# Kernel optimization log

Measured on AMD Instinct MI355X. Metric: run time of the kernel, lower is better.

## Reference

```python
import jax, jax.numpy as jnp
import numpy as np


def setup_inputs() -> dict:
    key = jax.random.key(0)
    x = jax.random.normal(key, (4, 512, 64, 64), dtype=jnp.float32)
    return {"x": x}


def reference(x) -> jnp.ndarray:
    B, C, H, W = x.shape
    N = H * W
    v = x.reshape(B, C, N)                      # proj_query/key/value all = x flattened
    # energy[b, i, j] = sum_c x[b,c,i] * x[b,c,j]
    energy = jnp.einsum('bci,bcj->bij', v, v)
    attention = jax.nn.softmax(energy, axis=-1)  # softmax over last dim (keys j)
    # out[b,c,i] = sum_j v[b,c,j] * attention[b,i,j]  (== V @ attention^T)
    out = jnp.einsum('bcj,bij->bci', v, attention)
    return out.reshape(B, C, H, W)
```

## Files before the change

### kernel.cpp

```cpp
#include <hip/hip_runtime.h>
#include <hip/hip_bf16.h>

typedef unsigned short u16;
typedef unsigned int   u32;
typedef unsigned long long u64;
typedef __attribute__((ext_vector_type(8))) short bf16x8;
typedef __attribute__((ext_vector_type(4))) float f32x4;

#define BB 4
#define CC 512
#define NN 4096
#define LOG2E 1.44269504f

static __device__ __forceinline__ u16 f2b(float f) {
    __hip_bfloat16 h = __float2bfloat16(f);
    return *(u16*)&h;
}
static __device__ __forceinline__ u16 f2b_fast(float f) {
    u32 u = __builtin_bit_cast(u32, f);
    return (u16)((u + 0x8000u) >> 16);
}
static __device__ __forceinline__ float b2f(u16 b) {
    u32 u = (u32)b << 16;
    return __builtin_bit_cast(float, u);
}

typedef __attribute__((address_space(1))) const u32 GU32;
typedef __attribute__((address_space(3))) u32 LU32;
__device__ __forceinline__ void async16(const void* g, void* l) {
    __builtin_amdgcn_global_load_lds((GU32*)g, (LU32*)l, 16, 0, 0);
}

__global__ __launch_bounds__(256) void prep_kernel(const float* __restrict__ x,
                                                   u16* __restrict__ XT,
                                                   u16* __restrict__ XN,
                                                   float* __restrict__ norms,
                                                   int* __restrict__ maxn) {
    __shared__ __align__(8) u16 tile[64][68];
    __shared__ float nsum[64];
    int blk = blockIdx.x;
    int b  = blk >> 6;
    int n0 = (blk & 63) << 6;
    int t  = threadIdx.x;
    if (t < 64) nsum[t] = 0.f;

    int nq    = t & 15;
    int rbase = t >> 4;
    float psum[4] = {0.f, 0.f, 0.f, 0.f};

    for (int c0 = 0; c0 < CC; c0 += 64) {
        #pragma unroll
        for (int p = 0; p < 4; ++p) {
            int cl = p * 16 + rbase;
            const float* src = x + ((size_t)(b * CC + c0 + cl) * NN) + n0 + nq * 4;
            float4 v = *(const float4*)src;
            psum[0] += v.x * v.x; psum[1] += v.y * v.y;
            psum[2] += v.z * v.z; psum[3] += v.w * v.w;
            u64 pk = (u64)f2b(v.x) | ((u64)f2b(v.y) << 16) |
                     ((u64)f2b(v.z) << 32) | ((u64)f2b(v.w) << 48);
            *(u64*)&XN[((size_t)(b * CC + c0 + cl) * NN) + n0 + nq * 4] = pk;
            *(u64*)&tile[cl][nq * 4] = pk;
        }
        __syncthreads();
        int c2 = (t & 31) * 2;
        int nb = t >> 5;
        #pragma unroll
        for (int rr = 0; rr < 8; ++rr) {
            int nl = rr * 8 + nb;
            u32 val = (u32)tile[c2][nl] | ((u32)tile[c2 + 1][nl] << 16);
            *(u32*)&XT[((size_t)(b * NN + n0 + nl) * CC) + c0 + c2] = val;
        }
        __syncthreads();
    }
    #pragma unroll
    for (int k = 0; k < 4; ++k) atomicAdd(&nsum[nq * 4 + k], psum[k]);
    __syncthreads();
    if (t < 64) {
        float v = nsum[t];
        norms[(size_t)b * NN + n0 + t] = v;
        float m = v;
        #pragma unroll
        for (int d = 1; d < 64; d <<= 1) m = fmaxf(m, __shfl_xor(m, d));
        if (t == 0) atomicMax(&maxn[b], __float_as_int(m));
    }
}

__global__ __launch_bounds__(256, 2) void flash_kernel(const u16* __restrict__ XT,
                                                       const u16* __restrict__ XN,
                                                       const float* __restrict__ norms,
                                                       const int* __restrict__ maxn,
                                                       float* __restrict__ outF,
                                                       u16* __restrict__ outH,
                                                       float* __restrict__ l0g,
                                                       float* __restrict__ l1g,
                                                       int split) {
    __shared__ __align__(16) u16 KtT[2][32 * 520];
    __shared__ __align__(16) u16 Plds[2][64 * 40];
    __shared__ float lLds[64];

    int blk   = blockIdx.x;
    int inner = blk & 255;
    int hf    = split ? (blk >> 8) : 0;
    int xcd = inner & 7;
    int b   = xcd >> 1;
    int ib  = (inner >> 3) + ((xcd & 1) << 5);
    int i_base = ib * 64;
    int jlo = hf * (NN / 2) * split;
    int njt = split ? 64 : 128;

    int t    = threadIdx.x;
    int w    = t >> 6;
    int lane = t & 63;
    int l15  = lane & 15;
    int q    = lane >> 4;

    const u16* xtb = XT + (size_t)b * NN * CC;
    const u16* xnb = XN + (size_t)b * CC * NN;

    float mxn = __int_as_float(maxn[b]);
    float M2[4];
    #pragma unroll
    for (int r = 0; r < 4; ++r) {
        float nr = norms[(size_t)b * NN + i_base + w * 16 + q * 4 + r];
        M2[r] = (sqrtf(nr * mxn) - 40.f) * LOG2E;
    }

    bf16x8 qf[16];
    {
        const u16* qrow = xtb + (size_t)(i_base + w * 16 + l15) * CC;
        #pragma unroll
        for (int kk = 0; kk < 16; ++kk)
            qf[kk] = *(const bf16x8*)(qrow + kk * 32 + q * 8);
    }

    f32x4 o[8][4];
    #pragma unroll
    for (int ct = 0; ct < 8; ++ct)
        #pragma unroll
        for (int it = 0; it < 4; ++it)
            o[ct][it] = (f32x4){0.f, 0.f, 0.f, 0.f};
    float lpart[4] = {0.f, 0.f, 0.f, 0.f};

    {
        const u16* src = xtb + (size_t)(jlo + w * 8) * CC + lane * 8;
        #pragma unroll
        for (int rr = 0; rr < 8; ++rr)
            async16(src + rr * CC, &KtT[0][(w * 8 + rr) * 520]);
    }
    __syncthreads();

    for (int jt = 0; jt < njt; ++jt) {
        int buf = jt & 1;
        int j0  = jlo + jt * 32;

        bf16x8 vf[8];
        #pragma unroll
        for (int ct = 0; ct < 8; ++ct)
            vf[ct] = *(const bf16x8*)(xnb + (size_t)(w * 128 + ct * 16 + l15) * NN + j0 + q * 8);

        if (jt + 1 < njt) {
            const u16* src = xtb + (size_t)(j0 + 32 + w * 8) * CC + lane * 8;
            #pragma unroll
            for (int rr = 0; rr < 8; ++rr)
                async16(src + rr * CC, &KtT[buf ^ 1][(w * 8 + rr) * 520]);
        }

        f32x4 s0 = {0.f,0.f,0.f,0.f}, s1 = {0.f,0.f,0.f,0.f};
        #pragma unroll
        for (int kk = 0; kk < 16; ++kk) {
            bf16x8 b0 = *(const bf16x8*)&KtT[buf][(l15)      * 520 + kk * 32 + q * 8];
            bf16x8 b1 = *(const bf16x8*)&KtT[buf][(16 + l15) * 520 + kk * 32 + q * 8];
            s0 = __builtin_amdgcn_mfma_f32_16x16x32_bf16(qf[kk], b0, s0, 0, 0, 0);
            s1 = __builtin_amdgcn_mfma_f32_16x16x32_bf16(qf[kk], b1, s1, 0, 0, 0);
        }

        #pragma unroll
        for (int r = 0; r < 4; ++r) {
            float p0 = __builtin_amdgcn_exp2f(fmaf(s0[r], LOG2E, -M2[r]));
            float p1 = __builtin_amdgcn_exp2f(fmaf(s1[r], LOG2E, -M2[r]));
            u16 h0 = f2b_fast(p0), h1 = f2b_fast(p1);
            lpart[r] += b2f(h0) + b2f(h1);
            int row = w * 16 + q * 4 + r;
            Plds[buf][row * 40 +      l15] = h0;
            Plds[buf][row * 40 + 16 + l15] = h1;
        }
        __syncthreads();

        bf16x8 pb[4];
        #pragma unroll
        for (int it = 0; it < 4; ++it)
            pb[it] = *(const bf16x8*)&Plds[buf][(it * 16 + l15) * 40 + q * 8];
        #pragma unroll
        for (int ct = 0; ct < 8; ++ct)
            #pragma unroll
            for (int it = 0; it < 4; ++it)
                o[ct][it] = __builtin_amdgcn_mfma_f32_16x16x32_bf16(vf[ct], pb[it], o[ct][it], 0, 0, 0);
    }

    #pragma unroll
    for (int r = 0; r < 4; ++r) {
        float s = lpart[r];
        s += __shfl_xor(s, 1);
        s += __shfl_xor(s, 2);
        s += __shfl_xor(s, 4);
        s += __shfl_xor(s, 8);
        lpart[r] = s;
    }

    if (!split) {
        if (l15 == 0) {
            #pragma unroll
            for (int r = 0; r < 4; ++r) lLds[w * 16 + q * 4 + r] = lpart[r];
        }
        __syncthreads();
        float linv[4];
        #pragma unroll
        for (int it = 0; it < 4; ++it) linv[it] = 1.f / lLds[it * 16 + l15];
        float* ob = outF + (size_t)b * CC * NN;
        #pragma unroll
        for (int ct = 0; ct < 8; ++ct)
            #pragma unroll
            for (int r = 0; r < 4; ++r) {
                int c = w * 128 + ct * 16 + q * 4 + r;
                float* orow = ob + (size_t)c * NN + i_base;
                #pragma unroll
                for (int it = 0; it < 4; ++it)
                    orow[it * 16 + l15] = o[ct][it][r] * linv[it];
            }
    } else {
        if (l15 == 0) {
            float* lg = (hf == 0) ? l0g : l1g;
            #pragma unroll
            for (int r = 0; r < 4; ++r)
                lg[(size_t)b * NN + i_base + w * 16 + q * 4 + r] = lpart[r];
        }
        if (hf == 0) {
            float* ob = outF + (size_t)b * CC * NN;
            #pragma unroll
            for (int ct = 0; ct < 8; ++ct)
                #pragma unroll
                for (int r = 0; r < 4; ++r) {
                    int c = w * 128 + ct * 16 + q * 4 + r;
                    float* orow = ob + (size_t)c * NN + i_base;
                    #pragma unroll
                    for (int it = 0; it < 4; ++it)
                        orow[it * 16 + l15] = o[ct][it][r];
                }
        } else {
            u16* ob = outH + (size_t)b * CC * NN;
            #pragma unroll
            for (int ct = 0; ct < 8; ++ct)
                #pragma unroll
                for (int r = 0; r < 4; ++r) {
                    int c = w * 128 + ct * 16 + q * 4 + r;
                    u16* orow = ob + (size_t)c * NN + i_base;
                    #pragma unroll
                    for (int it = 0; it < 4; ++it)
                        orow[it * 16 + l15] = f2b(o[ct][it][r]);
                }
        }
    }
}

__global__ __launch_bounds__(256) void combine_kernel(float* __restrict__ out,
                                                      const u16* __restrict__ P1,
                                                      const float* __restrict__ l0,
                                                      const float* __restrict__ l1) {
    size_t g = (size_t)blockIdx.x * 256 + threadIdx.x;
    size_t f = g * 4;
    int i = (int)(f & (NN - 1));
    int b = (int)(f >> 21);
    float4 p0 = *(float4*)&out[f];
    u64 pk = *(const u64*)&P1[f];
    float p0a[4] = {p0.x, p0.y, p0.z, p0.w};
    float r[4];
    #pragma unroll
    for (int k = 0; k < 4; ++k) {
        float l = l0[(size_t)b * NN + i + k] + l1[(size_t)b * NN + i + k];
        float p1f = b2f((u16)((pk >> (16 * k)) & 0xFFFFu));
        r[k] = (p0a[k] + p1f) / l;
    }
    *(float4*)&out[f] = (float4){r[0], r[1], r[2], r[3]};
}

extern "C" void kernel_launch(void* const* d_in, const int* in_sizes, int n_in,
                              void* d_out, int out_size, void* d_ws, size_t ws_size,
                              hipStream_t stream) {
    const float* x = (const float*)d_in[0];
    size_t SZ = (size_t)BB * NN * CC;
    u16* XT = (u16*)d_ws;
    u16* XN = XT + SZ;
    u16* P1 = XN + SZ;
    float* norms = (float*)(P1 + SZ);
    float* l0g   = norms + (size_t)BB * NN;
    float* l1g   = l0g + (size_t)BB * NN;
    int*   maxn  = (int*)(l1g + (size_t)BB * NN);
    size_t needed = 3 * SZ * 2 + 3 * (size_t)BB * NN * 4 + 64;
    int split = (ws_size >= needed) ? 1 : 0;
    float* out = (float*)d_out;
    if (!split) {
        norms = (float*)(XN + SZ);
        l0g = norms + (size_t)BB * NN;
        l1g = l0g;
        maxn = (int*)(l1g + (size_t)BB * NN);
    }

    hipMemsetAsync(maxn, 0, BB * sizeof(int), stream);
    prep_kernel<<<256, 256, 0, stream>>>(x, XT, XN, norms, maxn);
    if (split) {
        flash_kernel<<<512, 256, 0, stream>>>(XT, XN, norms, maxn, out, P1, l0g, l1g, 1);
        combine_kernel<<<(BB * CC * NN / 4) / 256, 256, 0, stream>>>(out, P1, l0g, l1g);
    } else {
        flash_kernel<<<256, 256, 0, stream>>>(XT, XN, norms, maxn, out, P1, l0g, l1g, 0);
    }
}
```

Baseline: 295.4 us.

## Split prep kernel across channel groups and add separate norm reduction kernel

The prep kernel used to launch 256 blocks that each looped over all 512 channels. It now launches 2048 blocks, one per (batch, channel group, position tile), and each block writes partial squared norms to a buffer. A new small kernel sums the 8 partials per position and computes the per-batch max norm, which replaces the memset and the global atomicMax. The transpose store is also widened to 64-bit writes. The aim is better occupancy and bandwidth in the prep phase, at the cost of one extra launch and an extra partial-norm buffer in the workspace.

```diff
diff --git a/kernel.cpp b/kernel.cpp
--- a/kernel.cpp
+++ b/kernel.cpp
@@ -34,54 +34,79 @@
 __global__ __launch_bounds__(256) void prep_kernel(const float* __restrict__ x,
                                                    u16* __restrict__ XT,
                                                    u16* __restrict__ XN,
-                                                   float* __restrict__ norms,
-                                                   int* __restrict__ maxn) {
+                                                   float* __restrict__ normp) {
     __shared__ __align__(8) u16 tile[64][68];
     __shared__ float nsum[64];
     int blk = blockIdx.x;
-    int b  = blk >> 6;
-    int n0 = (blk & 63) << 6;
+    int b  = blk >> 9;
+    int r2 = blk & 511;
+    int cg = r2 >> 6;
+    int c0 = cg << 6;
+    int n0 = (r2 & 63) << 6;
     int t  = threadIdx.x;
     if (t < 64) nsum[t] = 0.f;
 
     int nq    = t & 15;
     int rbase = t >> 4;
     float psum[4] = {0.f, 0.f, 0.f, 0.f};
-
-    for (int c0 = 0; c0 < CC; c0 += 64) {
-        #pragma unroll
-        for (int p = 0; p < 4; ++p) {
-            int cl = p * 16 + rbase;
-            const float* src = x + ((size_t)(b * CC + c0 + cl) * NN) + n0 + nq * 4;
-            float4 v = *(const float4*)src;
-            psum[0] += v.x * v.x; psum[1] += v.y * v.y;
-            psum[2] += v.z * v.z; psum[3] += v.w * v.w;
-            u64 pk = (u64)f2b(v.x) | ((u64)f2b(v.y) << 16) |
-                     ((u64)f2b(v.z) << 32) | ((u64)f2b(v.w) << 48);
-            *(u64*)&XN[((size_t)(b * CC + c0 + cl) * NN) + n0 + nq * 4] = pk;
-            *(u64*)&tile[cl][nq * 4] = pk;
-        }
-        __syncthreads();
-        int c2 = (t & 31) * 2;
-        int nb = t >> 5;
-        #pragma unroll
-        for (int rr = 0; rr < 8; ++rr) {
-            int nl = rr * 8 + nb;
-            u32 val = (u32)tile[c2][nl] | ((u32)tile[c2 + 1][nl] << 16);
-            *(u32*)&XT[((size_t)(b * NN + n0 + nl) * CC) + c0 + c2] = val;
-        }
-        __syncthreads();
+    #pragma unroll
+    for (int p = 0; p < 4; ++p) {
+        int cl = p * 16 + rbase;
+        const float* src = x + ((size_t)(b * CC + c0 + cl) * NN) + n0 + nq * 4;
+        float4 v = *(const float4*)src;
+        psum[0] += v.x * v.x; psum[1] += v.y * v.y;
+        psum[2] += v.z * v.z; psum[3] += v.w * v.w;
+        u64 pk = (u64)f2b(v.x) | ((u64)f2b(v.y) << 16) |
+                 ((u64)f2b(v.z) << 32) | ((u64)f2b(v.w) << 48);
+        *(u64*)&XN[((size_t)(b * CC + c0 + cl) * NN) + n0 + nq * 4] = pk;
+        *(u64*)&tile[cl][nq * 4] = pk;
+    }
+    __syncthreads();
+
+    {
+        int c4 = (t & 15) * 4;
+        int nb = t >> 4;
+        #pragma unroll
+        for (int rr = 0; rr < 4; ++rr) {
+            int nl = rr * 16 + nb;
+            u64 pk = (u64)tile[c4][nl] | ((u64)tile[c4 + 1][nl] << 16) |
+                     ((u64)tile[c4 + 2][nl] << 32) | ((u64)tile[c4 + 3][nl] << 48);
+            *(u64*)&XT[((size_t)(b * NN + n0 + nl) * CC) + c0 + c4] = pk;
+        }
     }
     #pragma unroll
     for (int k = 0; k < 4; ++k) atomicAdd(&nsum[nq * 4 + k], psum[k]);
     __syncthreads();
-    if (t < 64) {
-        float v = nsum[t];
-        norms[(size_t)b * NN + n0 + t] = v;
-        float m = v;
-        #pragma unroll
-        for (int d = 1; d < 64; d <<= 1) m = fmaxf(m, __shfl_xor(m, d));
-        if (t == 0) atomicMax(&maxn[b], __float_as_int(m));
+    if (t < 64)
+        normp[((size_t)cg * BB + b) * NN + n0 + t] = nsum[t];
+}
+
+__global__ __launch_bounds__(1024) void nred_kernel(const float* __restrict__ normp,
+                                                    float* __restrict__ norms,
+                                                    int* __restrict__ maxn) {
+    int b = blockIdx.x;
+    int t = threadIdx.x;
+    float m = 0.f;
+    #pragma unroll
+    for (int k = 0; k < 4; ++k) {
+        int n = k * 1024 + t;
+        float s = 0.f;
+        #pragma unroll
+        for (int cg = 0; cg < 8; ++cg)
+            s += normp[((size_t)cg * BB + b) * NN + n];
+        norms[(size_t)b * NN + n] = s;
+        m = fmaxf(m, s);
+    }
+    #pragma unroll
+    for (int d = 1; d < 64; d <<= 1) m = fmaxf(m, __shfl_xor(m, d));
+    __shared__ float wred[16];
+    if ((t & 63) == 0) wred[t >> 6] = m;
+    __syncthreads();
+    if (t < 16) {
+        float v = wred[t];
+        #pragma unroll
+        for (int d = 1; d < 16; d <<= 1) v = fmaxf(v, __shfl_xor(v, d));
+        if (t == 0) maxn[b] = __float_as_int(v);
     }
 }
 
@@ -288,25 +313,28 @@
                               hipStream_t stream) {
     const float* x = (const float*)d_in[0];
     size_t SZ = (size_t)BB * NN * CC;
+    size_t BN = (size_t)BB * NN;
     u16* XT = (u16*)d_ws;
     u16* XN = XT + SZ;
     u16* P1 = XN + SZ;
     float* norms = (float*)(P1 + SZ);
-    float* l0g   = norms + (size_t)BB * NN;
-    float* l1g   = l0g + (size_t)BB * NN;
-    int*   maxn  = (int*)(l1g + (size_t)BB * NN);
-    size_t needed = 3 * SZ * 2 + 3 * (size_t)BB * NN * 4 + 64;
+    float* l0g   = norms + BN;
+    float* l1g   = l0g + BN;
+    float* normp = l1g + BN;
+    int*   maxn  = (int*)(normp + 8 * BN);
+    size_t needed = 3 * SZ * 2 + 3 * BN * 4 + 8 * BN * 4 + 64;
     int split = (ws_size >= needed) ? 1 : 0;
     float* out = (float*)d_out;
     if (!split) {
         norms = (float*)(XN + SZ);
-        l0g = norms + (size_t)BB * NN;
+        l0g = norms + BN;
         l1g = l0g;
-        maxn = (int*)(l1g + (size_t)BB * NN);
-    }
-
-    hipMemsetAsync(maxn, 0, BB * sizeof(int), stream);
-    prep_kernel<<<256, 256, 0, stream>>>(x, XT, XN, norms, maxn);
+        normp = l1g + BN;
+        maxn = (int*)(normp + 8 * BN);
+    }
+
+    prep_kernel<<<2048, 256, 0, stream>>>(x, XT, XN, normp);
+    nred_kernel<<<BB, 1024, 0, stream>>>(normp, norms, maxn);
     if (split) {
         flash_kernel<<<512, 256, 0, stream>>>(XT, XN, norms, maxn, out, P1, l0g, l1g, 1);
         combine_kernel<<<(BB * CC * NN / 4) / 256, 256, 0, stream>>>(out, P1, l0g, l1g);
```

New measurement: 294.1 us. Within noise of the previous version (-0.5%).
